# Kernel optimization log

Hardware: AMD Instinct MI355X
Metric: run time of the kernel (lower is better)

Reference implementation:

```python
import jax, jax.numpy as jnp
import numpy as np

DIM = 128
HEADS = 4
DIM_HEAD = 32
BASE_SCALE = DIM_HEAD ** (-0.5)
EPS = 1e-5


def _ln(x, g, b):
    mu = jnp.mean(x, axis=-1, keepdims=True)
    var = jnp.mean((x - mu) ** 2, axis=-1, keepdims=True)
    return (x - mu) * jax.lax.rsqrt(var + EPS) * g + b


def setup_inputs() -> dict:
    key = jax.random.key(0)
    ks = jax.random.split(key, 16)
    B, N, X, Y, W1, W2, D = 2, 4, 16, 16, 8, 8, DIM
    C = HEADS * DIM_HEAD
    inp = {
        "q": jax.random.normal(ks[0], (B, N, X, Y, W1, W2, D), jnp.float32),
        "k": jax.random.normal(ks[1], (B, N, X, Y, W1, W2, D), jnp.float32),
        "v": jax.random.normal(ks[2], (B, N, X, Y, W1, W2, D), jnp.float32),
        "skip": jax.random.normal(ks[3], (B, X, Y, W1, W2, D), jnp.float32),
        # per-batch temperature in [0.5, 1.5) to avoid divide blowup
        "temperature": jax.random.uniform(ks[4], (B,), jnp.float32) + 0.5,
        "ln_q_g": jnp.ones((D,), jnp.float32),
        "ln_q_b": jnp.zeros((D,), jnp.float32),
        "ln_k_g": jnp.ones((D,), jnp.float32),
        "ln_k_b": jnp.zeros((D,), jnp.float32),
        "ln_v_g": jnp.ones((D,), jnp.float32),
        "ln_v_b": jnp.zeros((D,), jnp.float32),
        "wq": jax.random.normal(ks[5], (D, C), jnp.float32) * 0.02,
        "bq": jnp.zeros((C,), jnp.float32),
        "wk": jax.random.normal(ks[6], (D, C), jnp.float32) * 0.02,
        "bk": jnp.zeros((C,), jnp.float32),
        "wv": jax.random.normal(ks[7], (D, C), jnp.float32) * 0.02,
        "bv": jnp.zeros((C,), jnp.float32),
        "w_proj": jax.random.normal(ks[8], (C, D), jnp.float32) * 0.02,
        "b_proj": jnp.zeros((D,), jnp.float32),
    }
    return inp


def reference(q, k, v, skip, temperature,
              ln_q_g, ln_q_b, ln_k_g, ln_k_b, ln_v_g, ln_v_b,
              wq, bq, wk, bk, wv, bv, w_proj, b_proj):
    B, N, X, Y, W1, W2, D = q.shape
    L, T = X * Y, N * W1 * W2
    M, Dh = HEADS, DIM_HEAD

    def to_tokens(x):  # b n x y w1 w2 d -> b (x y) (n w1 w2) d
        return jnp.transpose(x, (0, 2, 3, 1, 4, 5, 6)).reshape(B, L, T, D)

    def proj_in(x, g, bb, W, bias):
        return _ln(to_tokens(x), g, bb) @ W + bias  # (B, L, T, M*Dh)

    def split_heads(x):  # channel index = m*Dh + d, heads slow
        return jnp.transpose(x.reshape(B, L, T, M, Dh), (0, 3, 1, 2, 4))  # (B,M,L,T,Dh)

    qh = split_heads(proj_in(q, ln_q_g, ln_q_b, wq, bq))
    kh = split_heads(proj_in(k, ln_k_g, ln_k_b, wk, bk))
    vh = split_heads(proj_in(v, ln_v_g, ln_v_b, wv, bv))

    scale = (BASE_SCALE / temperature)[:, None, None, None, None]  # per-batch, bcast over heads
    dot = jnp.einsum('bmlqd,bmlkd->bmlqk', qh * scale, kh)
    att = jax.nn.softmax(dot, axis=-1)
    a = jnp.einsum('bmlqk,bmlkd->bmlqd', att, vh)  # (B,M,L,T,Dh)

    a = jnp.transpose(a, (0, 2, 3, 1, 4)).reshape(B, L, T, M * Dh)
    a = a.reshape(B, X, Y, N, W1, W2, M * Dh)
    a = jnp.transpose(a, (0, 3, 1, 2, 4, 5, 6))  # b n x y w1 w2 c
    z = a @ w_proj + b_proj
    z = jnp.mean(z, axis=1)  # mean over views n
    return z + skip
```

## Files before the change

### kernel.cpp

```cpp
#include <hip/hip_runtime.h>


typedef unsigned short u16;
typedef unsigned int u32;
typedef short bf16x8 __attribute__((ext_vector_type(8)));
typedef float f32x4 __attribute__((ext_vector_type(4)));

__device__ __forceinline__ float bf2f(u16 u) {
  union { unsigned int i; float f; } v; v.i = ((unsigned int)u) << 16; return v.f;
}
__device__ __forceinline__ u16 f2bf(float f) {
  union { float f; unsigned int i; } v; v.f = f;
  unsigned int x = v.i;
  return (u16)((x + 0x7fffu + ((x >> 16) & 1u)) >> 16);
}

__global__ __launch_bounds__(256) void ln_proj_mfma(
    const float* __restrict__ xq, const float* __restrict__ xk, const float* __restrict__ xv,
    const float* __restrict__ g_q, const float* __restrict__ b_q,
    const float* __restrict__ g_k, const float* __restrict__ b_k,
    const float* __restrict__ g_v, const float* __restrict__ b_v,
    const float* __restrict__ wq, const float* __restrict__ bq,
    const float* __restrict__ wk, const float* __restrict__ bk,
    const float* __restrict__ wv, const float* __restrict__ bv,
    u16* __restrict__ Qp, u16* __restrict__ Kp, u16* __restrict__ VpT)
{
  __shared__ u16  Wt_s[128 * 136];
  __shared__ float S_s[128];
  __shared__ float B2_s[128];

  const float *xp, *gp, *bp, *Wp, *biasp;
  u16* outp;
  if (blockIdx.y == 0)      { xp = xq; gp = g_q; bp = b_q; Wp = wq; biasp = bq; outp = Qp; }
  else if (blockIdx.y == 1) { xp = xk; gp = g_k; bp = b_k; Wp = wk; biasp = bk; outp = Kp; }
  else                      { xp = xv; gp = g_v; bp = b_v; Wp = wv; biasp = bv; outp = VpT; }

  const int tid = threadIdx.x;

#pragma unroll
  for (int it = 0; it < 32; ++it) {
    int f = it * 256 + tid;
    int c = f & 127, d0 = (f >> 7) * 2;
    float w0 = Wp[d0 * 128 + c] * gp[d0];
    float w1 = Wp[(d0 + 1) * 128 + c] * gp[d0 + 1];
    u32 pk = (u32)f2bf(w0) | ((u32)f2bf(w1) << 16);
    *(u32*)&Wt_s[c * 136 + (d0 ^ ((c & 15) << 3))] = pk;
  }
  {
    int c = tid & 127;
    float accv = 0.f;
#pragma unroll 4
    for (int d = 0; d < 128; ++d) {
      float coef = (tid < 128) ? gp[d] : bp[d];
      accv += coef * Wp[d * 128 + c];
    }
    if (tid < 128) S_s[c] = accv;
    else           B2_s[c] = accv + biasp[c];
  }
  __syncthreads();

  const int lane = tid & 63, wv_ = tid >> 6;
  const int c0 = lane & 15, g = lane >> 4;

  for (int rnd = 0; rnd < 4; ++rnd) {
    const int tilebase = (blockIdx.x * 4 + rnd) * 2;
    bf16x8 xf[2][4];
    float mu[2], rsv[2];
    int tokv[2];
#pragma unroll
    for (int t = 0; t < 2; ++t) {
      int tok = (tilebase + t) * 64 + wv_ * 16 + c0;
      tokv[t] = tok;
      int tt = tok & 255, bl = tok >> 8;
      int l = bl & 255, bi = bl >> 8;
      int xx = l >> 4, yy = l & 15;
      int n = tt >> 6, w1 = (tt >> 3) & 7, w2 = tt & 7;
      int row = (((((bi * 4 + n) * 16 + xx) * 16 + yy) * 8 + w1) * 8 + w2) * 128;
      float s1 = 0.f, s2 = 0.f;
#pragma unroll
      for (int ks = 0; ks < 4; ++ks) {
        float4 lo = *(const float4*)(xp + row + ks * 32 + g * 8);
        float4 hi = *(const float4*)(xp + row + ks * 32 + g * 8 + 4);
        s1 += lo.x + lo.y + lo.z + lo.w + hi.x + hi.y + hi.z + hi.w;
        s2 += lo.x * lo.x + lo.y * lo.y + lo.z * lo.z + lo.w * lo.w
            + hi.x * hi.x + hi.y * hi.y + hi.z * hi.z + hi.w * hi.w;
        bf16x8 xv;
        xv[0] = (short)f2bf(lo.x); xv[1] = (short)f2bf(lo.y);
        xv[2] = (short)f2bf(lo.z); xv[3] = (short)f2bf(lo.w);
        xv[4] = (short)f2bf(hi.x); xv[5] = (short)f2bf(hi.y);
        xv[6] = (short)f2bf(hi.z); xv[7] = (short)f2bf(hi.w);
        xf[t][ks] = xv;
      }
      s1 += __shfl_xor(s1, 16); s2 += __shfl_xor(s2, 16);
      s1 += __shfl_xor(s1, 32); s2 += __shfl_xor(s2, 32);
      float m = s1 * (1.0f / 128.0f);
      float var = s2 * (1.0f / 128.0f) - m * m;
      mu[t] = m;
      rsv[t] = rsqrtf(var + 1e-5f);
    }
#pragma unroll
    for (int ct = 0; ct < 8; ++ct) {
      const int cb = ct * 16 + g * 4;
      float4 S4 = *(const float4*)&S_s[cb];
      float4 B4 = *(const float4*)&B2_s[cb];
      bf16x8 wf[4];
#pragma unroll
      for (int ks = 0; ks < 4; ++ks)
        wf[ks] = *(const bf16x8*)&Wt_s[(ct * 16 + c0) * 136 + ((ks * 32 + g * 8) ^ (c0 << 3))];
#pragma unroll
      for (int t = 0; t < 2; ++t) {
        f32x4 acc = {0.f, 0.f, 0.f, 0.f};
#pragma unroll
        for (int ks = 0; ks < 4; ++ks)
          acc = __builtin_amdgcn_mfma_f32_16x16x32_bf16(wf[ks], xf[t][ks], acc, 0, 0, 0);
        float z0 = rsv[t] * (acc[0] - mu[t] * S4.x) + B4.x;
        float z1 = rsv[t] * (acc[1] - mu[t] * S4.y) + B4.y;
        float z2 = rsv[t] * (acc[2] - mu[t] * S4.z) + B4.z;
        float z3 = rsv[t] * (acc[3] - mu[t] * S4.w) + B4.w;
        if (blockIdx.y == 2) {
          int head = (tokv[t] >> 8) * 4 + (cb >> 5);
          int dh0 = cb & 31, tcol = tokv[t] & 255;
          outp[(head * 32 + dh0 + 0) * 256 + tcol] = f2bf(z0);
          outp[(head * 32 + dh0 + 1) * 256 + tcol] = f2bf(z1);
          outp[(head * 32 + dh0 + 2) * 256 + tcol] = f2bf(z2);
          outp[(head * 32 + dh0 + 3) * 256 + tcol] = f2bf(z3);
        } else {
          ushort4 zv;
          zv.x = f2bf(z0); zv.y = f2bf(z1); zv.z = f2bf(z2); zv.w = f2bf(z3);
          *(ushort4*)(outp + tokv[t] * 128 + cb) = zv;
        }
      }
    }
  }
}

__global__ __launch_bounds__(256) void attn_mfma(
    u16* __restrict__ Qp, const u16* __restrict__ Kp, const u16* __restrict__ VpT,
    const float* __restrict__ temperature)
{
  __shared__ u16 K_s[256 * 32];
  __shared__ u16 Vt_s[32 * 256];
  __shared__ u16 P_s[4][16 * 64];

  const int tid = threadIdx.x;
  const int bid = blockIdx.x;
  const int l = bid & 255, m = (bid >> 8) & 3, b = bid >> 10;
  const float scale = 0.17677669529663689f / temperature[b];
  const int base = (b * 256 + l) * 32768 + m * 32;
  const int head = (b * 256 + l) * 4 + m;

#pragma unroll
  for (int r = 0; r < 8; ++r) {
    int f = r * 256 + tid, t = f >> 3, c4 = (f & 7) * 4;
    *(ushort4*)&K_s[t * 32 + c4] = *(const ushort4*)(Kp + base + t * 128 + c4);
  }
#pragma unroll
  for (int r = 0; r < 8; ++r) {
    int f = r * 256 + tid, dh = f >> 6, c4 = (f & 63) * 4;
    ushort4 vv = *(const ushort4*)(VpT + (head * 32 + dh) * 256 + c4);
    *(ushort4*)&Vt_s[dh * 256 + (c4 ^ ((dh & 7) << 3))] = vv;
  }
  __syncthreads();

  const int lane = tid & 63, wv_ = tid >> 6;
  const int c0 = lane & 15, g = lane >> 4;
  u16* Pw = P_s[wv_];
  const f32x4 zero = {0.f, 0.f, 0.f, 0.f};

  for (int si = 0; si < 4; ++si) {
    const int qs = wv_ * 4 + si;
    bf16x8 qf = *(const bf16x8*)(Qp + base + (qs * 16 + c0) * 128 + g * 8);
    float p0 = 0.f, p1 = 0.f, p2 = 0.f, p3 = 0.f;
    f32x4 o0 = zero, o1 = zero;
    const int r0 = g * 4;
#pragma unroll 1
    for (int cc = 0; cc < 4; ++cc) {
      f32x4 s[4];
#pragma unroll
      for (int kt = 0; kt < 4; ++kt) {
        bf16x8 kf = *(const bf16x8*)&K_s[((cc * 4 + kt) * 16 + c0) * 32 + g * 8];
        s[kt] = __builtin_amdgcn_mfma_f32_16x16x32_bf16(qf, kf, zero, 0, 0, 0);
      }
#pragma unroll
      for (int kt = 0; kt < 4; ++kt) {
        float e0 = __expf(s[kt][0] * scale);
        float e1 = __expf(s[kt][1] * scale);
        float e2 = __expf(s[kt][2] * scale);
        float e3 = __expf(s[kt][3] * scale);
        p0 += e0; p1 += e1; p2 += e2; p3 += e3;
        int col = kt * 16 + c0;
        Pw[(r0 + 0) * 64 + (col ^ (((r0 + 0) & 7) << 3))] = f2bf(e0);
        Pw[(r0 + 1) * 64 + (col ^ (((r0 + 1) & 7) << 3))] = f2bf(e1);
        Pw[(r0 + 2) * 64 + (col ^ (((r0 + 2) & 7) << 3))] = f2bf(e2);
        Pw[(r0 + 3) * 64 + (col ^ (((r0 + 3) & 7) << 3))] = f2bf(e3);
      }
#pragma unroll
      for (int kc = 0; kc < 2; ++kc) {
        bf16x8 af = *(const bf16x8*)&Pw[c0 * 64 + ((kc * 32 + g * 8) ^ ((c0 & 7) << 3))];
        int Kg = cc * 64 + kc * 32 + g * 8;
        bf16x8 v0 = *(const bf16x8*)&Vt_s[c0 * 256 + (Kg ^ ((c0 & 7) << 3))];
        bf16x8 v1 = *(const bf16x8*)&Vt_s[(16 + c0) * 256 + (Kg ^ ((c0 & 7) << 3))];
        o0 = __builtin_amdgcn_mfma_f32_16x16x32_bf16(af, v0, o0, 0, 0, 0);
        o1 = __builtin_amdgcn_mfma_f32_16x16x32_bf16(af, v1, o1, 0, 0, 0);
      }
    }
#pragma unroll
    for (int off = 1; off <= 8; off <<= 1) {
      p0 += __shfl_xor(p0, off);
      p1 += __shfl_xor(p1, off);
      p2 += __shfl_xor(p2, off);
      p3 += __shfl_xor(p3, off);
    }
    float inv0 = 1.0f / p0, inv1 = 1.0f / p1, inv2 = 1.0f / p2, inv3 = 1.0f / p3;
    int qrow = qs * 16 + g * 4;
    Qp[base + (qrow + 0) * 128 + c0]      = f2bf(o0[0] * inv0);
    Qp[base + (qrow + 1) * 128 + c0]      = f2bf(o0[1] * inv1);
    Qp[base + (qrow + 2) * 128 + c0]      = f2bf(o0[2] * inv2);
    Qp[base + (qrow + 3) * 128 + c0]      = f2bf(o0[3] * inv3);
    Qp[base + (qrow + 0) * 128 + 16 + c0] = f2bf(o1[0] * inv0);
    Qp[base + (qrow + 1) * 128 + 16 + c0] = f2bf(o1[1] * inv1);
    Qp[base + (qrow + 2) * 128 + 16 + c0] = f2bf(o1[2] * inv2);
    Qp[base + (qrow + 3) * 128 + 16 + c0] = f2bf(o1[3] * inv3);
  }
}

__global__ __launch_bounds__(256) void out_proj_mfma(
    const u16* __restrict__ Ap, const float* __restrict__ wp, const float* __restrict__ bpr,
    const float* __restrict__ skip, float* __restrict__ out)
{
  __shared__ u16 WpT_s[128 * 136];
  const int tid = threadIdx.x;
#pragma unroll
  for (int it = 0; it < 32; ++it) {
    int f = it * 256 + tid;
    int c = f & 127, d0 = (f >> 7) * 2;
    float w0 = wp[d0 * 128 + c] * 0.25f;
    float w1 = wp[(d0 + 1) * 128 + c] * 0.25f;
    u32 pk = (u32)f2bf(w0) | ((u32)f2bf(w1) << 16);
    *(u32*)&WpT_s[c * 136 + (d0 ^ ((c & 15) << 3))] = pk;
  }
  __syncthreads();

  const int lane = tid & 63, wv_ = tid >> 6;
  const int c0 = lane & 15, g = lane >> 4;
  const int bl = blockIdx.x;
  const int w = wv_ * 16 + c0;
  const int otok = bl * 64 + w;

  bf16x8 bfr[4];
#pragma unroll
  for (int ks = 0; ks < 4; ++ks) {
    float acc8[8] = {0.f, 0.f, 0.f, 0.f, 0.f, 0.f, 0.f, 0.f};
#pragma unroll
    for (int n = 0; n < 4; ++n) {
      bf16x8 a = *(const bf16x8*)(Ap + (bl * 256 + n * 64 + w) * 128 + ks * 32 + g * 8);
#pragma unroll
      for (int e = 0; e < 8; ++e) acc8[e] += bf2f((u16)a[e]);
    }
    bf16x8 r;
#pragma unroll
    for (int e = 0; e < 8; ++e) r[e] = (short)f2bf(acc8[e]);
    bfr[ks] = r;
  }
#pragma unroll
  for (int ct = 0; ct < 8; ++ct) {
    f32x4 acc = {0.f, 0.f, 0.f, 0.f};
#pragma unroll
    for (int ks = 0; ks < 4; ++ks) {
      bf16x8 wf = *(const bf16x8*)&WpT_s[(ct * 16 + c0) * 136 + ((ks * 32 + g * 8) ^ (c0 << 3))];
      acc = __builtin_amdgcn_mfma_f32_16x16x32_bf16(wf, bfr[ks], acc, 0, 0, 0);
    }
    int d0 = ct * 16 + g * 4;
    int ob = otok * 128 + d0;
    float4 sk = *(const float4*)(skip + ob);
    float4 b4 = *(const float4*)(bpr + d0);
    float4 zv;
    zv.x = acc[0] + b4.x + sk.x;
    zv.y = acc[1] + b4.y + sk.y;
    zv.z = acc[2] + b4.z + sk.z;
    zv.w = acc[3] + b4.w + sk.w;
    *(float4*)(out + ob) = zv;
  }
}

extern "C" void kernel_launch(void* const* d_in, const int* in_sizes, int n_in,
                              void* d_out, int out_size, void* d_ws, size_t ws_size,
                              hipStream_t stream)
{
  (void)in_sizes; (void)n_in; (void)out_size; (void)ws_size;
  const float* q    = (const float*)d_in[0];
  const float* k    = (const float*)d_in[1];
  const float* v    = (const float*)d_in[2];
  const float* skip = (const float*)d_in[3];
  const float* temp = (const float*)d_in[4];
  const float* gq   = (const float*)d_in[5];
  const float* bq_l = (const float*)d_in[6];
  const float* gk   = (const float*)d_in[7];
  const float* bk_l = (const float*)d_in[8];
  const float* gv   = (const float*)d_in[9];
  const float* bv_l = (const float*)d_in[10];
  const float* wq   = (const float*)d_in[11];
  const float* bq   = (const float*)d_in[12];
  const float* wk   = (const float*)d_in[13];
  const float* bk   = (const float*)d_in[14];
  const float* wv   = (const float*)d_in[15];
  const float* bv   = (const float*)d_in[16];
  const float* wp   = (const float*)d_in[17];
  const float* bp   = (const float*)d_in[18];
  float* out = (float*)d_out;

  const size_t S = (size_t)2 * 256 * 256 * 128;
  u16* Qp  = (u16*)d_ws;
  u16* Kp  = Qp + S;
  u16* VpT = Kp + S;

  ln_proj_mfma<<<dim3(256, 3), 256, 0, stream>>>(
      q, k, v, gq, bq_l, gk, bk_l, gv, bv_l,
      wq, bq, wk, bk, wv, bv, Qp, Kp, VpT);
  attn_mfma<<<dim3(2048), 256, 0, stream>>>(Qp, Kp, VpT, temp);
  out_proj_mfma<<<dim3(512), 256, 0, stream>>>(Qp, wp, bp, skip, out);
}
```

Baseline: 348.8 us.

## Precompute bf16 weight images once and launch one token tile per block

Adds two small setup kernels that build the gamma-scaled, swizzled bf16 weight images and the LN bias/sum vectors once per call in workspace. The projection and output kernels then copy these images into shared memory instead of recomputing them in every block. The projection kernel now uses one 64-token tile per block with 2048×3 blocks instead of looping over 8 tiles, which gives more parallelism but adds a per-block image copy. The f2bf helper also switches to the compiler's native bf16 conversion, and the change adds two extra kernel launches.

```diff
diff --git a/kernel.cpp b/kernel.cpp
--- a/kernel.cpp
+++ b/kernel.cpp
@@ -10,9 +10,59 @@
   union { unsigned int i; float f; } v; v.i = ((unsigned int)u) << 16; return v.f;
 }
 __device__ __forceinline__ u16 f2bf(float f) {
-  union { float f; unsigned int i; } v; v.f = f;
-  unsigned int x = v.i;
-  return (u16)((x + 0x7fffu + ((x >> 16) & 1u)) >> 16);
+  __bf16 h = (__bf16)f;
+  u16 r; __builtin_memcpy(&r, &h, 2); return r;
+}
+
+#define IMG_ELEMS (128 * 136)
+
+__global__ __launch_bounds__(256) void setup_sb(
+    const float* __restrict__ g_q, const float* __restrict__ b_q,
+    const float* __restrict__ g_k, const float* __restrict__ b_k,
+    const float* __restrict__ g_v, const float* __restrict__ b_v,
+    const float* __restrict__ wq, const float* __restrict__ bq,
+    const float* __restrict__ wk, const float* __restrict__ bk,
+    const float* __restrict__ wv, const float* __restrict__ bv,
+    float* __restrict__ Sg, float* __restrict__ B2g)
+{
+  const float *gp, *bp, *Wp, *biasp;
+  int y = blockIdx.x;
+  if (y == 0)      { gp = g_q; bp = b_q; Wp = wq; biasp = bq; }
+  else if (y == 1) { gp = g_k; bp = b_k; Wp = wk; biasp = bk; }
+  else             { gp = g_v; bp = b_v; Wp = wv; biasp = bv; }
+  int c = threadIdx.x & 127;
+  float acc = 0.f;
+#pragma unroll 8
+  for (int d = 0; d < 128; ++d) {
+    float coef = (threadIdx.x < 128) ? gp[d] : bp[d];
+    acc += coef * Wp[d * 128 + c];
+  }
+  if (threadIdx.x < 128) Sg[y * 128 + c] = acc;
+  else                   B2g[y * 128 + c] = acc + biasp[c];
+}
+
+__global__ __launch_bounds__(256) void setup_w(
+    const float* __restrict__ g_q, const float* __restrict__ g_k, const float* __restrict__ g_v,
+    const float* __restrict__ wq, const float* __restrict__ wk, const float* __restrict__ wv,
+    const float* __restrict__ wp, u16* __restrict__ imgs)
+{
+  int y = blockIdx.y;
+  const float* Wp; const float* gp = nullptr; float mul = 1.f;
+  if (y == 0)      { Wp = wq; gp = g_q; }
+  else if (y == 1) { Wp = wk; gp = g_k; }
+  else if (y == 2) { Wp = wv; gp = g_v; }
+  else             { Wp = wp; mul = 0.25f; }
+  u16* img = imgs + y * IMG_ELEMS;
+#pragma unroll
+  for (int it = 0; it < 4; ++it) {
+    int f = (blockIdx.x * 4 + it) * 256 + threadIdx.x;
+    int c = f & 127, d0 = (f >> 7) * 2;
+    float m0 = gp ? gp[d0] : mul, m1 = gp ? gp[d0 + 1] : mul;
+    float w0 = Wp[d0 * 128 + c] * m0;
+    float w1 = Wp[(d0 + 1) * 128 + c] * m1;
+    u32 pk = (u32)f2bf(w0) | ((u32)f2bf(w1) << 16);
+    *(u32*)&img[c * 136 + (d0 ^ ((c & 15) << 3))] = pk;
+  }
 }
 
 __global__ __launch_bounds__(256) void ln_proj_mfma(
@@ -23,30 +73,34 @@
     const float* __restrict__ wq, const float* __restrict__ bq,
     const float* __restrict__ wk, const float* __restrict__ bk,
     const float* __restrict__ wv, const float* __restrict__ bv,
+    const u16* __restrict__ imgs, const float* __restrict__ Sg, const float* __restrict__ B2g,
     u16* __restrict__ Qp, u16* __restrict__ Kp, u16* __restrict__ VpT)
 {
-  __shared__ u16  Wt_s[128 * 136];
-  __shared__ float S_s[128];
-  __shared__ float B2_s[128];
-
+  __shared__ u16   Wt_s[IMG_ELEMS];
+  __shared__ float S_s[128], B2_s[128];
+
+  const int y = blockIdx.y, tid = threadIdx.x;
   const float *xp, *gp, *bp, *Wp, *biasp;
   u16* outp;
-  if (blockIdx.y == 0)      { xp = xq; gp = g_q; bp = b_q; Wp = wq; biasp = bq; outp = Qp; }
-  else if (blockIdx.y == 1) { xp = xk; gp = g_k; bp = b_k; Wp = wk; biasp = bk; outp = Kp; }
-  else                      { xp = xv; gp = g_v; bp = b_v; Wp = wv; biasp = bv; outp = VpT; }
-
-  const int tid = threadIdx.x;
-
-#pragma unroll
-  for (int it = 0; it < 32; ++it) {
-    int f = it * 256 + tid;
-    int c = f & 127, d0 = (f >> 7) * 2;
-    float w0 = Wp[d0 * 128 + c] * gp[d0];
-    float w1 = Wp[(d0 + 1) * 128 + c] * gp[d0 + 1];
-    u32 pk = (u32)f2bf(w0) | ((u32)f2bf(w1) << 16);
-    *(u32*)&Wt_s[c * 136 + (d0 ^ ((c & 15) << 3))] = pk;
-  }
-  {
+  if (y == 0)      { xp = xq; gp = g_q; bp = b_q; Wp = wq; biasp = bq; outp = Qp; }
+  else if (y == 1) { xp = xk; gp = g_k; bp = b_k; Wp = wk; biasp = bk; outp = Kp; }
+  else             { xp = xv; gp = g_v; bp = b_v; Wp = wv; biasp = bv; outp = VpT; }
+
+  if (imgs) {
+    const int4* src = (const int4*)(imgs + y * IMG_ELEMS);
+    int4* dst = (int4*)Wt_s;
+#pragma unroll
+    for (int i = 0; i < 17; ++i) dst[i * 256 + tid] = src[i * 256 + tid];
+    if (tid < 128) S_s[tid] = Sg[y * 128 + tid];
+    else           B2_s[tid - 128] = B2g[y * 128 + (tid - 128)];
+  } else {
+    for (int it = 0; it < 32; ++it) {
+      int c = it * 4 + (tid >> 6), d0 = (tid & 63) * 2;
+      float w0 = Wp[d0 * 128 + c] * gp[d0];
+      float w1 = Wp[(d0 + 1) * 128 + c] * gp[d0 + 1];
+      u32 pk = (u32)f2bf(w0) | ((u32)f2bf(w1) << 16);
+      *(u32*)&Wt_s[c * 136 + (d0 ^ ((c & 15) << 3))] = pk;
+    }
     int c = tid & 127;
     float accv = 0.f;
 #pragma unroll 4
@@ -62,74 +116,61 @@
   const int lane = tid & 63, wv_ = tid >> 6;
   const int c0 = lane & 15, g = lane >> 4;
 
-  for (int rnd = 0; rnd < 4; ++rnd) {
-    const int tilebase = (blockIdx.x * 4 + rnd) * 2;
-    bf16x8 xf[2][4];
-    float mu[2], rsv[2];
-    int tokv[2];
-#pragma unroll
-    for (int t = 0; t < 2; ++t) {
-      int tok = (tilebase + t) * 64 + wv_ * 16 + c0;
-      tokv[t] = tok;
-      int tt = tok & 255, bl = tok >> 8;
-      int l = bl & 255, bi = bl >> 8;
-      int xx = l >> 4, yy = l & 15;
-      int n = tt >> 6, w1 = (tt >> 3) & 7, w2 = tt & 7;
-      int row = (((((bi * 4 + n) * 16 + xx) * 16 + yy) * 8 + w1) * 8 + w2) * 128;
-      float s1 = 0.f, s2 = 0.f;
-#pragma unroll
-      for (int ks = 0; ks < 4; ++ks) {
-        float4 lo = *(const float4*)(xp + row + ks * 32 + g * 8);
-        float4 hi = *(const float4*)(xp + row + ks * 32 + g * 8 + 4);
-        s1 += lo.x + lo.y + lo.z + lo.w + hi.x + hi.y + hi.z + hi.w;
-        s2 += lo.x * lo.x + lo.y * lo.y + lo.z * lo.z + lo.w * lo.w
-            + hi.x * hi.x + hi.y * hi.y + hi.z * hi.z + hi.w * hi.w;
-        bf16x8 xv;
-        xv[0] = (short)f2bf(lo.x); xv[1] = (short)f2bf(lo.y);
-        xv[2] = (short)f2bf(lo.z); xv[3] = (short)f2bf(lo.w);
-        xv[4] = (short)f2bf(hi.x); xv[5] = (short)f2bf(hi.y);
-        xv[6] = (short)f2bf(hi.z); xv[7] = (short)f2bf(hi.w);
-        xf[t][ks] = xv;
-      }
-      s1 += __shfl_xor(s1, 16); s2 += __shfl_xor(s2, 16);
-      s1 += __shfl_xor(s1, 32); s2 += __shfl_xor(s2, 32);
-      float m = s1 * (1.0f / 128.0f);
-      float var = s2 * (1.0f / 128.0f) - m * m;
-      mu[t] = m;
-      rsv[t] = rsqrtf(var + 1e-5f);
-    }
-#pragma unroll
-    for (int ct = 0; ct < 8; ++ct) {
-      const int cb = ct * 16 + g * 4;
-      float4 S4 = *(const float4*)&S_s[cb];
-      float4 B4 = *(const float4*)&B2_s[cb];
-      bf16x8 wf[4];
-#pragma unroll
-      for (int ks = 0; ks < 4; ++ks)
-        wf[ks] = *(const bf16x8*)&Wt_s[(ct * 16 + c0) * 136 + ((ks * 32 + g * 8) ^ (c0 << 3))];
-#pragma unroll
-      for (int t = 0; t < 2; ++t) {
-        f32x4 acc = {0.f, 0.f, 0.f, 0.f};
-#pragma unroll
-        for (int ks = 0; ks < 4; ++ks)
-          acc = __builtin_amdgcn_mfma_f32_16x16x32_bf16(wf[ks], xf[t][ks], acc, 0, 0, 0);
-        float z0 = rsv[t] * (acc[0] - mu[t] * S4.x) + B4.x;
-        float z1 = rsv[t] * (acc[1] - mu[t] * S4.y) + B4.y;
-        float z2 = rsv[t] * (acc[2] - mu[t] * S4.z) + B4.z;
-        float z3 = rsv[t] * (acc[3] - mu[t] * S4.w) + B4.w;
-        if (blockIdx.y == 2) {
-          int head = (tokv[t] >> 8) * 4 + (cb >> 5);
-          int dh0 = cb & 31, tcol = tokv[t] & 255;
-          outp[(head * 32 + dh0 + 0) * 256 + tcol] = f2bf(z0);
-          outp[(head * 32 + dh0 + 1) * 256 + tcol] = f2bf(z1);
-          outp[(head * 32 + dh0 + 2) * 256 + tcol] = f2bf(z2);
-          outp[(head * 32 + dh0 + 3) * 256 + tcol] = f2bf(z3);
-        } else {
-          ushort4 zv;
-          zv.x = f2bf(z0); zv.y = f2bf(z1); zv.z = f2bf(z2); zv.w = f2bf(z3);
-          *(ushort4*)(outp + tokv[t] * 128 + cb) = zv;
-        }
-      }
+  const int tok = blockIdx.x * 64 + wv_ * 16 + c0;
+  const int tt = tok & 255, bl = tok >> 8;
+  const int l = bl & 255, bi = bl >> 8;
+  const int xx = l >> 4, yy = l & 15;
+  const int n = tt >> 6, w1_ = (tt >> 3) & 7, w2 = tt & 7;
+  const int row = (((((bi * 4 + n) * 16 + xx) * 16 + yy) * 8 + w1_) * 8 + w2) * 128;
+
+  float s1 = 0.f, s2 = 0.f;
+  bf16x8 xf[4];
+#pragma unroll
+  for (int ks = 0; ks < 4; ++ks) {
+    float4 lo = *(const float4*)(xp + row + ks * 32 + g * 8);
+    float4 hi = *(const float4*)(xp + row + ks * 32 + g * 8 + 4);
+    s1 += lo.x + lo.y + lo.z + lo.w + hi.x + hi.y + hi.z + hi.w;
+    s2 += lo.x * lo.x + lo.y * lo.y + lo.z * lo.z + lo.w * lo.w
+        + hi.x * hi.x + hi.y * hi.y + hi.z * hi.z + hi.w * hi.w;
+    bf16x8 xv;
+    xv[0] = (short)f2bf(lo.x); xv[1] = (short)f2bf(lo.y);
+    xv[2] = (short)f2bf(lo.z); xv[3] = (short)f2bf(lo.w);
+    xv[4] = (short)f2bf(hi.x); xv[5] = (short)f2bf(hi.y);
+    xv[6] = (short)f2bf(hi.z); xv[7] = (short)f2bf(hi.w);
+    xf[ks] = xv;
+  }
+  s1 += __shfl_xor(s1, 16); s2 += __shfl_xor(s2, 16);
+  s1 += __shfl_xor(s1, 32); s2 += __shfl_xor(s2, 32);
+  const float mu = s1 * (1.0f / 128.0f);
+  const float var = s2 * (1.0f / 128.0f) - mu * mu;
+  const float rs = rsqrtf(var + 1e-5f);
+
+#pragma unroll
+  for (int ct = 0; ct < 8; ++ct) {
+    const int cb = ct * 16 + g * 4;
+    f32x4 acc = {0.f, 0.f, 0.f, 0.f};
+#pragma unroll
+    for (int ks = 0; ks < 4; ++ks) {
+      bf16x8 wf = *(const bf16x8*)&Wt_s[(ct * 16 + c0) * 136 + ((ks * 32 + g * 8) ^ (c0 << 3))];
+      acc = __builtin_amdgcn_mfma_f32_16x16x32_bf16(wf, xf[ks], acc, 0, 0, 0);
+    }
+    float4 S4 = *(const float4*)&S_s[cb];
+    float4 B4 = *(const float4*)&B2_s[cb];
+    float z0 = rs * (acc[0] - mu * S4.x) + B4.x;
+    float z1 = rs * (acc[1] - mu * S4.y) + B4.y;
+    float z2 = rs * (acc[2] - mu * S4.z) + B4.z;
+    float z3 = rs * (acc[3] - mu * S4.w) + B4.w;
+    if (y == 2) {
+      int head = (tok >> 8) * 4 + (cb >> 5);
+      int dh0 = cb & 31, tcol = tok & 255;
+      outp[(head * 32 + dh0 + 0) * 256 + tcol] = f2bf(z0);
+      outp[(head * 32 + dh0 + 1) * 256 + tcol] = f2bf(z1);
+      outp[(head * 32 + dh0 + 2) * 256 + tcol] = f2bf(z2);
+      outp[(head * 32 + dh0 + 3) * 256 + tcol] = f2bf(z3);
+    } else {
+      ushort4 zv;
+      zv.x = f2bf(z0); zv.y = f2bf(z1); zv.z = f2bf(z2); zv.w = f2bf(z3);
+      *(ushort4*)(outp + tok * 128 + cb) = zv;
     }
   }
 }
@@ -225,19 +266,25 @@
 }
 
 __global__ __launch_bounds__(256) void out_proj_mfma(
-    const u16* __restrict__ Ap, const float* __restrict__ wp, const float* __restrict__ bpr,
+    const u16* __restrict__ Ap, const u16* __restrict__ img3,
+    const float* __restrict__ wp, const float* __restrict__ bpr,
     const float* __restrict__ skip, float* __restrict__ out)
 {
-  __shared__ u16 WpT_s[128 * 136];
+  __shared__ u16 WpT_s[IMG_ELEMS];
   const int tid = threadIdx.x;
-#pragma unroll
-  for (int it = 0; it < 32; ++it) {
-    int f = it * 256 + tid;
-    int c = f & 127, d0 = (f >> 7) * 2;
-    float w0 = wp[d0 * 128 + c] * 0.25f;
-    float w1 = wp[(d0 + 1) * 128 + c] * 0.25f;
-    u32 pk = (u32)f2bf(w0) | ((u32)f2bf(w1) << 16);
-    *(u32*)&WpT_s[c * 136 + (d0 ^ ((c & 15) << 3))] = pk;
+  if (img3) {
+    const int4* src = (const int4*)img3;
+    int4* dst = (int4*)WpT_s;
+#pragma unroll
+    for (int i = 0; i < 17; ++i) dst[i * 256 + tid] = src[i * 256 + tid];
+  } else {
+    for (int it = 0; it < 32; ++it) {
+      int c = it * 4 + (tid >> 6), d0 = (tid & 63) * 2;
+      float w0 = wp[d0 * 128 + c] * 0.25f;
+      float w1 = wp[(d0 + 1) * 128 + c] * 0.25f;
+      u32 pk = (u32)f2bf(w0) | ((u32)f2bf(w1) << 16);
+      *(u32*)&WpT_s[c * 136 + (d0 ^ ((c & 15) << 3))] = pk;
+    }
   }
   __syncthreads();
 
@@ -287,7 +334,7 @@
                               void* d_out, int out_size, void* d_ws, size_t ws_size,
                               hipStream_t stream)
 {
-  (void)in_sizes; (void)n_in; (void)out_size; (void)ws_size;
+  (void)in_sizes; (void)n_in; (void)out_size;
   const float* q    = (const float*)d_in[0];
   const float* k    = (const float*)d_in[1];
   const float* v    = (const float*)d_in[2];
@@ -313,10 +360,23 @@
   u16* Qp  = (u16*)d_ws;
   u16* Kp  = Qp + S;
   u16* VpT = Kp + S;
-
-  ln_proj_mfma<<<dim3(256, 3), 256, 0, stream>>>(
+  u16* imgs = VpT + S;
+  float* Sg  = (float*)(imgs + 4 * IMG_ELEMS);
+  float* B2g = Sg + 3 * 128;
+
+  const size_t need = (size_t)3 * S * 2 + (size_t)4 * IMG_ELEMS * 2 + 6 * 128 * 4;
+  const bool pre = (ws_size >= need);
+
+  if (pre) {
+    setup_sb<<<dim3(3), 256, 0, stream>>>(gq, bq_l, gk, bk_l, gv, bv_l,
+                                          wq, bq, wk, bk, wv, bv, Sg, B2g);
+    setup_w<<<dim3(8, 4), 256, 0, stream>>>(gq, gk, gv, wq, wk, wv, wp, imgs);
+  }
+  ln_proj_mfma<<<dim3(2048, 3), 256, 0, stream>>>(
       q, k, v, gq, bq_l, gk, bk_l, gv, bv_l,
-      wq, bq, wk, bk, wv, bv, Qp, Kp, VpT);
+      wq, bq, wk, bk, wv, bv,
+      pre ? imgs : (const u16*)nullptr, Sg, B2g, Qp, Kp, VpT);
   attn_mfma<<<dim3(2048), 256, 0, stream>>>(Qp, Kp, VpT, temp);
-  out_proj_mfma<<<dim3(512), 256, 0, stream>>>(Qp, wp, bp, skip, out);
-}
+  out_proj_mfma<<<dim3(512), 256, 0, stream>>>(
+      Qp, pre ? (imgs + 3 * IMG_ELEMS) : (const u16*)nullptr, wp, bp, skip, out);
+}
```

Measured after the change: 331.8 us. 1.05x faster.
